# Optimization experiments

Hardware: AMD Instinct MI355X
Metric: run time of the kernel (lower is better)

Reference implementation:

```python
import jax, jax.numpy as jnp
import numpy as np
import math

D_MODEL = 1024
NUM_HEADS = 16
D_K = D_MODEL // NUM_HEADS
B, NQ, NK = 2, 2048, 2048


def setup_inputs() -> dict:
    key = jax.random.key(0)
    ks = jax.random.split(key, 14)
    s = 1.0 / math.sqrt(D_MODEL)
    inp = {
        "query": jax.random.normal(ks[0], (B, NQ, D_MODEL), jnp.float32),
        "key": jax.random.normal(ks[1], (B, NK, D_MODEL), jnp.float32),
        "value": jax.random.normal(ks[2], (B, NK, D_MODEL), jnp.float32),
        "mask": jax.random.randint(ks[3], (B, NK), 0, 2, jnp.int32),
        "attn_bias": jax.random.normal(ks[4], (B, NQ, NK), jnp.float32),
        "w_q": jax.random.normal(ks[5], (D_MODEL, D_MODEL), jnp.float32) * s,
        "b_q": jnp.zeros((D_MODEL,), jnp.float32),
        "w_k": jax.random.normal(ks[6], (D_MODEL, D_MODEL), jnp.float32) * s,
        "b_k": jnp.zeros((D_MODEL,), jnp.float32),
        "w_v": jax.random.normal(ks[7], (D_MODEL, D_MODEL), jnp.float32) * s,
        "b_v": jnp.zeros((D_MODEL,), jnp.float32),
        "w_o": jax.random.normal(ks[8], (D_MODEL, D_MODEL), jnp.float32) * s,
        "b_o": jnp.zeros((D_MODEL,), jnp.float32),
    }
    return inp


def reference(query, key, value, mask, attn_bias, w_q, b_q, w_k, b_k, w_v, b_v, w_o, b_o):
    # Linear projections (torch Linear: x @ W^T + b), reshape to [B, H, N, d_k]
    def proj(x, w, b, n):
        return (x @ w.T + b).reshape(x.shape[0], n, NUM_HEADS, D_K).transpose(0, 2, 1, 3)

    Q = proj(query, w_q, b_q, query.shape[1])   # [B,H,Nq,dk]
    K = proj(key, w_k, b_k, key.shape[1])       # [B,H,Nk,dk]
    V = proj(value, w_v, b_v, value.shape[1])   # [B,H,Nk,dk]

    scores = jnp.einsum("bhqd,bhkd->bhqk", Q, K) / math.sqrt(D_K)
    scores = scores + attn_bias[:, None, :, :]           # bias broadcast over heads
    pad = (mask[:, None, None, :] == 0)                   # [B,1,1,Nk]
    scores = jnp.where(pad, jnp.float32(-1e9), scores)
    attn = jax.nn.softmax(scores, axis=-1)                # dropout is identity (eval)
    out = jnp.einsum("bhqk,bhkd->bhqd", attn, V)          # [B,H,Nq,dk]
    out = out.transpose(0, 2, 1, 3).reshape(query.shape[0], query.shape[1], D_MODEL)
    return out @ w_o.T + b_o
```

## Files before the change

kernel.cpp:

```cpp
#include <hip/hip_runtime.h>


typedef short bf16x8 __attribute__((ext_vector_type(8)));
typedef short bf16x4 __attribute__((ext_vector_type(4)));
typedef float f32x4 __attribute__((ext_vector_type(4)));
typedef float f32x16 __attribute__((ext_vector_type(16)));
typedef int i32x4 __attribute__((ext_vector_type(4)));
typedef unsigned short u16;
typedef unsigned short u16x8 __attribute__((ext_vector_type(8)));
typedef unsigned short u16x4 __attribute__((ext_vector_type(4)));

#define MFMA16(a, b, c) __builtin_amdgcn_mfma_f32_16x16x32_bf16((a), (b), (c), 0, 0, 0)
#define MFMA32(a, b, c) __builtin_amdgcn_mfma_f32_32x32x16_bf16((a), (b), (c), 0, 0, 0)
#define GLD16(gp, lp)                                                     \
  __builtin_amdgcn_global_load_lds(                                       \
      (const __attribute__((address_space(1))) void*)(gp),                \
      (__attribute__((address_space(3))) void*)(lp), 16, 0, 0)

#define WAITVM_BAR(N) asm volatile("s_waitcnt vmcnt(" #N ")\ns_barrier" ::: "memory")
#define BAR() asm volatile("s_barrier" ::: "memory")

#if __has_builtin(__builtin_amdgcn_exp2f)
#define EXP2(x) __builtin_amdgcn_exp2f(x)
#else
#define EXP2(x) exp2f(x)
#endif

__device__ __forceinline__ u16 f2bf(float f) {
  union { float f; unsigned u; } v; v.f = f;
  return (u16)((v.u + 0x7fffu + ((v.u >> 16) & 1u)) >> 16);
}
__device__ __forceinline__ unsigned pk2(float x, float y) {
  union { float f; unsigned u; } a, b;
  a.f = x; b.f = y;
  return ((a.u + 0x8000u) >> 16) | ((b.u + 0x8000u) & 0xffff0000u);
}
__device__ __forceinline__ void pl32swap(unsigned& a, unsigned& b) {
  asm("v_permlane32_swap_b32 %0, %1" : "+v"(a), "+v"(b));
}

struct ConvDesc { const float* src; u16* dst; int n; };
struct ConvArgs { ConvDesc d[7]; };

__device__ __forceinline__ void biasprep_body(const float* __restrict__ bias,
                                              const int* __restrict__ mask,
                                              u16* __restrict__ out, int i) {
  const int o0 = i * 16;
  const int rowg = o0 >> 11;
  const int b = rowg >> 11;
  const int off = o0 & 2047;
  const int c = off >> 5;
  const int hi = (off >> 4) & 1;
  const float* src = bias + (size_t)rowg * 2048 + c * 32 + hi * 4;
  const int* msk = mask + b * 2048 + c * 32 + hi * 4;
  u16x8 w0 = {}, w1 = {};
#pragma unroll
  for (int t = 0; t < 4; t++) {
    f32x4 v = *(const f32x4*)(src + t * 8);
    i32x4 m = *(const i32x4*)(msk + t * 8);
#pragma unroll
    for (int j = 0; j < 4; j++) {
      u16 val = (m[j] != 0) ? f2bf(v[j] * 1.44269504f) : (u16)0xFF80;
      if (t < 2) w0[t * 4 + j] = val;
      else       w1[(t - 2) * 4 + j] = val;
    }
  }
  *(u16x8*)(out + o0) = w0;
  *(u16x8*)(out + o0 + 8) = w1;
}

__global__ __launch_bounds__(256)
void k_prep(ConvArgs a, const float* __restrict__ bias,
            const int* __restrict__ mask, u16* __restrict__ bout) {
  if (blockIdx.y == 7) {
    biasprep_body(bias, mask, bout, blockIdx.x * 256 + threadIdx.x);
    return;
  }
  ConvDesc cd = a.d[blockIdx.y];
  int i = (blockIdx.x * 256 + threadIdx.x) * 8;
  if (i >= cd.n) return;
  const float4* s = (const float4*)(cd.src + i);
  float4 f0 = s[0], f1 = s[1];
  u16x8 o;
  o[0] = f2bf(f0.x); o[1] = f2bf(f0.y); o[2] = f2bf(f0.z); o[3] = f2bf(f0.w);
  o[4] = f2bf(f1.x); o[5] = f2bf(f1.y); o[6] = f2bf(f1.z); o[7] = f2bf(f1.w);
  *(u16x8*)(cd.dst + i) = o;
}

__global__ __launch_bounds__(256)
void k_biasprep(const float* __restrict__ bias, const int* __restrict__ mask,
                u16* __restrict__ out) {
  biasprep_body(bias, mask, out, blockIdx.x * 256 + threadIdx.x);
}

template <int MF>
__device__ __forceinline__ void gemm_impl(const u16* __restrict__ A,
                                          const u16* __restrict__ Bw,
                                          const float* __restrict__ bias,
                                          void* __restrict__ outp, int mode,
                                          float oscale) {
  __shared__ u16 As[2][MF * 1024];
  __shared__ u16 Bs[2][4096];
  const int tid = threadIdx.x;
  const int lane = tid & 63;
  const int wv = tid >> 6;
  const int wr = wv >> 1, wc = wv & 1;
  const int m0 = blockIdx.y * (MF * 32), n0 = blockIdx.x * 128;

  f32x4 acc[MF][4] = {};

  const int s0 = tid, s1 = 256 + tid;
  const int r0 = s0 >> 2, c0 = (s0 & 3) ^ (r0 & 3);
  const int r1 = s1 >> 2, c1 = (s1 & 3) ^ (r1 & 3);
  const u16* gA0 = A + (size_t)(m0 + r0) * 1024 + c0 * 8;
  const u16* gA1 = A + (size_t)(m0 + r1) * 1024 + c1 * 8;
  const u16* gB0 = Bw + (size_t)(n0 + r0) * 1024 + c0 * 8;
  const u16* gB1 = Bw + (size_t)(n0 + r1) * 1024 + c1 * 8;
  u16* lA0 = &As[0][(tid & ~63) * 8];
  u16* lB0 = &Bs[0][(tid & ~63) * 8];

  GLD16(gA0, lA0);
  if constexpr (MF == 4) GLD16(gA1, lA0 + 2048);
  GLD16(gB0, lB0);
  GLD16(gB1, lB0 + 2048);
  WAITVM_BAR(0);

#define GSTEP(BUF, K0)                                                     \
  {                                                                        \
    const int nk = ((K0) + 32) & 1023;                                     \
    GLD16(gA0 + nk, lA0 + ((BUF) ^ 1) * (MF * 1024));                      \
    if constexpr (MF == 4)                                                 \
      GLD16(gA1 + nk, lA0 + 2048 + ((BUF) ^ 1) * (MF * 1024));             \
    GLD16(gB0 + nk, lB0 + ((BUF) ^ 1) * 4096);                             \
    GLD16(gB1 + nk, lB0 + 2048 + ((BUF) ^ 1) * 4096);                      \
    if constexpr (MF == 4) { WAITVM_BAR(4); } else { WAITVM_BAR(3); }      \
    bf16x8 af[MF], bfr[4];                                                 \
    _Pragma("unroll")                                                      \
    for (int mi = 0; mi < MF; mi++) {                                      \
      int row = wr * (MF * 16) + mi * 16 + (lane & 15);                    \
      int byt = row * 64 + (((lane >> 4) * 16) ^ ((row & 3) << 4));        \
      af[mi] = *(const bf16x8*)((const char*)&As[BUF][0] + byt);           \
    }                                                                      \
    _Pragma("unroll")                                                      \
    for (int ni = 0; ni < 4; ni++) {                                       \
      int row = wc * 64 + ni * 16 + (lane & 15);                           \
      int byt = row * 64 + (((lane >> 4) * 16) ^ ((row & 3) << 4));        \
      bfr[ni] = *(const bf16x8*)((const char*)&Bs[BUF][0] + byt);          \
    }                                                                      \
    __builtin_amdgcn_s_setprio(1);                                         \
    _Pragma("unroll")                                                      \
    for (int mi = 0; mi < MF; mi++)                                        \
      _Pragma("unroll")                                                    \
      for (int ni = 0; ni < 4; ni++)                                       \
        acc[mi][ni] = MFMA16(af[mi], bfr[ni], acc[mi][ni]);                \
    __builtin_amdgcn_s_setprio(0);                                         \
    BAR();                                                                 \
  }

  for (int k0 = 0; k0 < 1024; k0 += 64) {
    GSTEP(0, k0)
    GSTEP(1, k0 + 32)
  }
#undef GSTEP

#pragma unroll
  for (int ni = 0; ni < 4; ni++) {
    int n = n0 + wc * 64 + ni * 16 + (lane & 15);
    float bv = bias[n];
#pragma unroll
    for (int mi = 0; mi < MF; mi++) {
      int mb = m0 + wr * (MF * 16) + mi * 16 + (lane >> 4) * 4;
      if (mode == 2) {
        float* O = (float*)outp;
#pragma unroll
        for (int r = 0; r < 4; r++)
          O[(size_t)(mb + r) * 1024 + n] = (acc[mi][ni][r] + bv) * oscale;
      } else if (mode == 0) {
        u16* O = (u16*)outp;
        int b = mb >> 11, q = mb & 2047;
        int h = n >> 6, dk = n & 63;
        size_t base = ((size_t)(b * 16 + h) * 2048 + q) * 64 + dk;
#pragma unroll
        for (int r = 0; r < 4; r++)
          O[base + (size_t)r * 64] = f2bf((acc[mi][ni][r] + bv) * oscale);
      } else {
        u16* O = (u16*)outp;
        int b = mb >> 11, kv = mb & 2047;
        int h = n >> 6, dk = n & 63;
        u16x4 pk;
#pragma unroll
        for (int r = 0; r < 4; r++) pk[r] = f2bf((acc[mi][ni][r] + bv) * oscale);
        *(u16x4*)((u16*)O + ((size_t)((b * 16 + h) * 64 + dk)) * 2048 + kv) = pk;
      }
    }
  }
}

struct GemmDesc { const u16* A; const u16* W; const float* bias; void* out;
                  int mode; float oscale; };
struct Gemm3 { GemmDesc d[3]; };

__global__ __launch_bounds__(256, 2) void k_gemm_qkv(Gemm3 g3) {
  GemmDesc gd = g3.d[blockIdx.z];
  gemm_impl<4>(gd.A, gd.W, gd.bias, gd.out, gd.mode, gd.oscale);
}
__global__ __launch_bounds__(256, 2)
void k_gemm_o(const u16* __restrict__ A, const u16* __restrict__ W,
              const float* __restrict__ bias, float* __restrict__ out) {
  gemm_impl<2>(A, W, bias, out, 2, 1.0f);
}

__global__ __launch_bounds__(256, 2)
void k_attn(const u16* __restrict__ Qb, const u16* __restrict__ Kb,
            const u16* __restrict__ Vt, const u16* __restrict__ BiasE,
            u16* __restrict__ Ob) {
  __shared__ u16 Ks[2][128 * 64];
  __shared__ u16 Vs[2][64 * 128];

  const int tid = threadIdx.x, lane = tid & 63, w = tid >> 6;
  const int l31 = lane & 31, hi2 = lane >> 5;
  const int bid = blockIdx.x;
  const int xcd = bid & 7, rr = bid >> 3;
  const int qt = rr & 15;
  const int pr = xcd + 8 * (rr >> 4);
  const int b = pr >> 4, h = pr & 15;
  const int q0 = qt * 128;
  const size_t bh = (size_t)(b * 16 + h);

  const u16* Qrow = Qb + (bh * 2048 + q0 + w * 32 + l31) * 64 + hi2 * 8;
  bf16x8 bq[4];
#pragma unroll
  for (int dc = 0; dc < 4; dc++) bq[dc] = *(const bf16x8*)(Qrow + dc * 16);

  f32x16 acc[2] = {};
  float mrun = -1e30f, lrun = 0.f;

  const u16* Kg = Kb + bh * 2048 * 64;
  const u16* Vg = Vt + bh * 64 * 2048;
  int rK[4], cK[4], rV[4], cV[4], ldd[4];
#pragma unroll
  for (int i = 0; i < 4; i++) {
    int s = i * 256 + tid;
    rK[i] = s >> 3; cK[i] = (s & 7) ^ (rK[i] & 7);
    rV[i] = s >> 4; cV[i] = (s & 15) ^ (rV[i] & 7);
    ldd[i] = (i * 256 + (tid & ~63)) * 8;
  }
  const int kx = (lane & 7) << 4;

  const u16* brow =
      BiasE + ((size_t)b * 2048 + q0 + w * 32 + l31) * 2048 + hi2 * 16;

#pragma unroll
  for (int i = 0; i < 4; i++)
    GLD16(Kg + (size_t)rK[i] * 64 + cK[i] * 8, &Ks[0][ldd[i]]);
#pragma unroll
  for (int i = 0; i < 4; i++)
    GLD16(Vg + (size_t)rV[i] * 2048 + cV[i] * 8, &Vs[0][ldd[i]]);
  u16x8 bb[4][2];
#pragma unroll
  for (int c = 0; c < 4; c++) {
    bb[c][0] = *(const u16x8*)(brow + c * 32);
    bb[c][1] = *(const u16x8*)(brow + c * 32 + 8);
  }

#define ATTN_STEP(BUF, T)                                                      \
  {                                                                            \
    WAITVM_BAR(0);            \
    const char* kb = (const char*)&Ks[BUF][0];                                 \
    const char* vb = (const char*)&Vs[BUF][0];                                 \
    f32x16 sc[4];                                                              \
    __builtin_amdgcn_s_setprio(1);                                             \
    _Pragma("unroll")                                                          \
    for (int c = 0; c < 4; c++) {                                              \
      f32x16 z;                                                                \
      _Pragma("unroll")                                                        \
      for (int r = 0; r < 8; r++)                                              \
        z[r] = __uint_as_float((unsigned)bb[c][0][r] << 16);                   \
      _Pragma("unroll")                                                        \
      for (int r = 0; r < 8; r++)                                              \
        z[8 + r] = __uint_as_float((unsigned)bb[c][1][r] << 16);               \
      const int rowb = (c * 32 + l31) * 128;                                   \
      _Pragma("unroll")                                                        \
      for (int dc = 0; dc < 4; dc++) {                                         \
        bf16x8 ak =                                                            \
            *(const bf16x8*)(kb + rowb + ((dc * 32 + hi2 * 16) ^ kx));         \
        z = MFMA32(ak, bq[dc], z);                                             \
      }                                                                        \
      sc[c] = z;                                                               \
    }                                                                          \
    __builtin_amdgcn_s_setprio(0);                                             \
    const int nkv = (((T) + 1) & 15) * 128;                                    \
    _Pragma("unroll")                                                          \
    for (int i = 0; i < 4; i++)                                                \
      GLD16(Kg + (size_t)(nkv + rK[i]) * 64 + cK[i] * 8,                       \
            &Ks[(BUF) ^ 1][ldd[i]]);                                           \
    _Pragma("unroll")                                                          \
    for (int i = 0; i < 4; i++)                                                \
      GLD16(Vg + (size_t)rV[i] * 2048 + nkv + cV[i] * 8,                       \
            &Vs[(BUF) ^ 1][ldd[i]]);                                           \
    _Pragma("unroll")                                                          \
    for (int c = 0; c < 4; c++) {                                              \
      bb[c][0] = *(const u16x8*)(brow + nkv + c * 32);                         \
      bb[c][1] = *(const u16x8*)(brow + nkv + c * 32 + 8);                     \
    }                                                                          \
    float tmax = -3e38f;                                                       \
    _Pragma("unroll")                                                          \
    for (int c = 0; c < 4; c++)                                                \
      _Pragma("unroll")                                                        \
      for (int r = 0; r < 16; r++) tmax = fmaxf(tmax, sc[c][r]);               \
    tmax = fmaxf(tmax, __shfl_xor(tmax, 32, 64));                              \
    if (__any(tmax > mrun)) {                                                  \
      float mnew = fmaxf(mrun, tmax);                                          \
      float alpha = EXP2(mrun - mnew);                                         \
      mrun = mnew;                                                             \
      lrun *= alpha;                                                           \
      _Pragma("unroll")                                                        \
      for (int ds = 0; ds < 2; ds++)                                           \
        _Pragma("unroll")                                                      \
        for (int r = 0; r < 16; r++) acc[ds][r] *= alpha;                      \
    }                                                                          \
    float rsum = 0.f;                                                          \
    _Pragma("unroll")                                                          \
    for (int c = 0; c < 4; c++)                                                \
      _Pragma("unroll")                                                        \
      for (int r = 0; r < 16; r++) {                                           \
        sc[c][r] = EXP2(sc[c][r] - mrun);                                      \
        rsum += sc[c][r];                                                      \
      }                                                                        \
    rsum += __shfl_xor(rsum, 32, 64);                                          \
    lrun += rsum;                                                              \
    __builtin_amdgcn_s_setprio(1);                                             \
    _Pragma("unroll")                                                          \
    for (int c = 0; c < 4; c++) {                                              \
      unsigned a0 = pk2(sc[c][0], sc[c][1]), b0 = pk2(sc[c][4], sc[c][5]);     \
      unsigned a1 = pk2(sc[c][2], sc[c][3]), b1 = pk2(sc[c][6], sc[c][7]);     \
      unsigned e0 = pk2(sc[c][8], sc[c][9]), f0 = pk2(sc[c][12], sc[c][13]);   \
      unsigned e1 = pk2(sc[c][10], sc[c][11]), f1 = pk2(sc[c][14], sc[c][15]); \
      pl32swap(a0, b0); pl32swap(a1, b1);                                      \
      pl32swap(e0, f0); pl32swap(e1, f1);                                      \
      union { unsigned u[4]; bf16x8 v; } fe, fo;                               \
      fe.u[0] = a0; fe.u[1] = a1; fe.u[2] = b0; fe.u[3] = b1;                  \
      fo.u[0] = e0; fo.u[1] = e1; fo.u[2] = f0; fo.u[3] = f1;                  \
      _Pragma("unroll")                                                        \
      for (int ds = 0; ds < 2; ds++) {                                         \
        const int vrow = (ds * 32 + l31) * 256;                                \
        bf16x8 ve =                                                            \
            *(const bf16x8*)(vb + vrow + (((c * 4 + hi2) * 16) ^ kx));         \
        acc[ds] = MFMA32(ve, fe.v, acc[ds]);                                   \
        bf16x8 vo =                                                            \
            *(const bf16x8*)(vb + vrow + (((c * 4 + 2 + hi2) * 16) ^ kx));     \
        acc[ds] = MFMA32(vo, fo.v, acc[ds]);                                   \
      }                                                                        \
    }                                                                          \
    __builtin_amdgcn_s_setprio(0);                                             \
  }

  for (int t = 0; t < 16; t += 2) {
    ATTN_STEP(0, t)
    ATTN_STEP(1, t + 1)
  }
#undef ATTN_STEP

  float linv = 1.0f / lrun;
  const size_t obase =
      ((size_t)b * 2048 + q0 + w * 32 + l31) * 1024 + h * 64 + hi2 * 4;
#pragma unroll
  for (int ds = 0; ds < 2; ds++)
#pragma unroll
    for (int t = 0; t < 4; t++) {
      u16x4 pk;
#pragma unroll
      for (int j = 0; j < 4; j++) pk[j] = f2bf(acc[ds][t * 4 + j] * linv);
      *(u16x4*)(Ob + obase + ds * 32 + t * 8) = pk;
    }
}

extern "C" void kernel_launch(void* const* d_in, const int* in_sizes, int n_in,
                              void* d_out, int out_size, void* d_ws,
                              size_t ws_size, hipStream_t stream) {
  (void)in_sizes; (void)n_in; (void)out_size;
  const float* q_in = (const float*)d_in[0];
  const float* k_in = (const float*)d_in[1];
  const float* v_in = (const float*)d_in[2];
  const int* mask = (const int*)d_in[3];
  const float* attn_bias = (const float*)d_in[4];
  const float* w_q = (const float*)d_in[5];
  const float* b_q = (const float*)d_in[6];
  const float* w_k = (const float*)d_in[7];
  const float* b_k = (const float*)d_in[8];
  const float* w_v = (const float*)d_in[9];
  const float* b_v = (const float*)d_in[10];
  const float* w_o = (const float*)d_in[11];
  const float* b_o = (const float*)d_in[12];

  const size_t MB = 1u << 20;
  char* ws = (char*)d_ws;
  u16* XQ = (u16*)(ws + 0 * MB);
  u16* XK = (u16*)(ws + 8 * MB);
  u16* XV = (u16*)(ws + 16 * MB);
  u16* WQ = (u16*)(ws + 24 * MB);
  u16* WK = (u16*)(ws + 26 * MB);
  u16* WV = (u16*)(ws + 28 * MB);
  u16* WO = (u16*)(ws + 30 * MB);
  u16* Qb = (u16*)(ws + 32 * MB);
  u16* Kb = (u16*)(ws + 40 * MB);
  u16* Vt = (u16*)(ws + 48 * MB);
  u16* Ob = (u16*)(ws + 56 * MB);
  const bool merged = ws_size >= (size_t)80 * MB;
  u16* BiasE = (u16*)(ws + (merged ? 64 : 0) * MB);

  ConvArgs ca;
  ca.d[0] = {q_in, XQ, 4096 * 1024};
  ca.d[1] = {k_in, XK, 4096 * 1024};
  ca.d[2] = {v_in, XV, 4096 * 1024};
  ca.d[3] = {w_q, WQ, 1024 * 1024};
  ca.d[4] = {w_k, WK, 1024 * 1024};
  ca.d[5] = {w_v, WV, 1024 * 1024};
  ca.d[6] = {w_o, WO, 1024 * 1024};
  k_prep<<<dim3(2048, merged ? 8 : 7), 256, 0, stream>>>(ca, attn_bias, mask,
                                                         BiasE);

  const float QSCALE = 0.125f * 1.44269504f;
  Gemm3 g3;
  g3.d[0] = {XQ, WQ, b_q, (void*)Qb, 0, QSCALE};
  g3.d[1] = {XK, WK, b_k, (void*)Kb, 0, 1.0f};
  g3.d[2] = {XV, WV, b_v, (void*)Vt, 1, 1.0f};
  k_gemm_qkv<<<dim3(8, 32, 3), 256, 0, stream>>>(g3);

  if (!merged) k_biasprep<<<2048, 256, 0, stream>>>(attn_bias, mask, BiasE);

  k_attn<<<512, 256, 0, stream>>>(Qb, Kb, Vt, BiasE, Ob);

  k_gemm_o<<<dim3(8, 64), 256, 0, stream>>>(Ob, WO, b_o, (float*)d_out);
}
```

Measured before the change: 149.3 us.

## Tune attention softmax: tree reductions, lazy rescale, hardware bf16 pack, QKV occupancy

Several independent tweaks land together. The row-max and row-sum in the attention inner loop become tree reductions using three-input max, which shortens dependency chains. The running-max rescale now fires only when the new max exceeds the old by more than 8 (log2 units), which skips most accumulator rescales but lets exponentials reach up to 2^8 before rescale. Manual bf16 packing is replaced with the HIP __float22bfloat162_rn intrinsic, which may map to a hardware convert instruction. The QKV GEMM launch bound is raised to 3 blocks per SM, which can force register spills.

After: 147.4 us. Within noise of the previous version (-1.2%).

```diff
diff --git a/kernel.cpp b/kernel.cpp
--- a/kernel.cpp
+++ b/kernel.cpp
@@ -1,4 +1,5 @@
 #include <hip/hip_runtime.h>
+#include <hip/hip_bf16.h>
 
 
 typedef short bf16x8 __attribute__((ext_vector_type(8)));
@@ -30,10 +31,10 @@
   union { float f; unsigned u; } v; v.f = f;
   return (u16)((v.u + 0x7fffu + ((v.u >> 16) & 1u)) >> 16);
 }
-__device__ __forceinline__ unsigned pk2(float x, float y) {
-  union { float f; unsigned u; } a, b;
-  a.f = x; b.f = y;
-  return ((a.u + 0x8000u) >> 16) | ((b.u + 0x8000u) & 0xffff0000u);
+__device__ __forceinline__ unsigned pkc(float lo, float hi) {
+  __hip_bfloat162 h = __float22bfloat162_rn(float2{lo, hi});
+  union { __hip_bfloat162 h; unsigned u; } c; c.h = h;
+  return c.u;
 }
 __device__ __forceinline__ void pl32swap(unsigned& a, unsigned& b) {
   asm("v_permlane32_swap_b32 %0, %1" : "+v"(a), "+v"(b));
@@ -200,7 +201,7 @@
                   int mode; float oscale; };
 struct Gemm3 { GemmDesc d[3]; };
 
-__global__ __launch_bounds__(256, 2) void k_gemm_qkv(Gemm3 g3) {
+__global__ __launch_bounds__(256, 3) void k_gemm_qkv(Gemm3 g3) {
   GemmDesc gd = g3.d[blockIdx.z];
   gemm_impl<4>(gd.A, gd.W, gd.bias, gd.out, gd.mode, gd.oscale);
 }
@@ -303,13 +304,20 @@
       bb[c][0] = *(const u16x8*)(brow + nkv + c * 32);                         \
       bb[c][1] = *(const u16x8*)(brow + nkv + c * 32 + 8);                     \
     }                                                                          \
-    float tmax = -3e38f;                                                       \
-    _Pragma("unroll")                                                          \
-    for (int c = 0; c < 4; c++)                                                \
-      _Pragma("unroll")                                                        \
-      for (int r = 0; r < 16; r++) tmax = fmaxf(tmax, sc[c][r]);               \
+    float cm[4];                                                               \
+    _Pragma("unroll")                                                          \
+    for (int c = 0; c < 4; c++) {     \
+      float qa = fmaxf(fmaxf(sc[c][0], sc[c][1]), sc[c][2]);                   \
+      float qb = fmaxf(fmaxf(sc[c][3], sc[c][4]), sc[c][5]);                   \
+      float qc = fmaxf(fmaxf(sc[c][6], sc[c][7]), sc[c][8]);                   \
+      float qd = fmaxf(fmaxf(sc[c][9], sc[c][10]), sc[c][11]);                 \
+      float qe = fmaxf(fmaxf(sc[c][12], sc[c][13]), sc[c][14]);                \
+      cm[c] = fmaxf(fmaxf(fmaxf(qa, qb), fmaxf(qc, qd)),                       \
+                    fmaxf(qe, sc[c][15]));                                     \
+    }                                                                          \
+    float tmax = fmaxf(fmaxf(cm[0], cm[1]), fmaxf(cm[2], cm[3]));              \
     tmax = fmaxf(tmax, __shfl_xor(tmax, 32, 64));                              \
-    if (__any(tmax > mrun)) {                                                  \
+    if (__any(tmax > mrun + 8.f)) {           \
       float mnew = fmaxf(mrun, tmax);                                          \
       float alpha = EXP2(mrun - mnew);                                         \
       mrun = mnew;                                                             \
@@ -319,23 +327,31 @@
         _Pragma("unroll")                                                      \
         for (int r = 0; r < 16; r++) acc[ds][r] *= alpha;                      \
     }                                                                          \
-    float rsum = 0.f;                                                          \
     _Pragma("unroll")                                                          \
     for (int c = 0; c < 4; c++)                                                \
       _Pragma("unroll")                                                        \
-      for (int r = 0; r < 16; r++) {                                           \
-        sc[c][r] = EXP2(sc[c][r] - mrun);                                      \
-        rsum += sc[c][r];                                                      \
-      }                                                                        \
+      for (int r = 0; r < 16; r++) sc[c][r] = EXP2(sc[c][r] - mrun);           \
+    float cs[4];                                                               \
+    _Pragma("unroll")                                                          \
+    for (int c = 0; c < 4; c++) {                                              \
+      float s8[8];                                                             \
+      _Pragma("unroll")                                                        \
+      for (int r = 0; r < 8; r++) s8[r] = sc[c][r] + sc[c][r + 8];             \
+      float s4[4];                                                             \
+      _Pragma("unroll")                                                        \
+      for (int r = 0; r < 4; r++) s4[r] = s8[r] + s8[r + 4];                   \
+      cs[c] = (s4[0] + s4[1]) + (s4[2] + s4[3]);                               \
+    }                                                                          \
+    float rsum = (cs[0] + cs[1]) + (cs[2] + cs[3]);                            \
     rsum += __shfl_xor(rsum, 32, 64);                                          \
     lrun += rsum;                                                              \
     __builtin_amdgcn_s_setprio(1);                                             \
     _Pragma("unroll")                                                          \
     for (int c = 0; c < 4; c++) {                                              \
-      unsigned a0 = pk2(sc[c][0], sc[c][1]), b0 = pk2(sc[c][4], sc[c][5]);     \
-      unsigned a1 = pk2(sc[c][2], sc[c][3]), b1 = pk2(sc[c][6], sc[c][7]);     \
-      unsigned e0 = pk2(sc[c][8], sc[c][9]), f0 = pk2(sc[c][12], sc[c][13]);   \
-      unsigned e1 = pk2(sc[c][10], sc[c][11]), f1 = pk2(sc[c][14], sc[c][15]); \
+      unsigned a0 = pkc(sc[c][0], sc[c][1]), b0 = pkc(sc[c][4], sc[c][5]);     \
+      unsigned a1 = pkc(sc[c][2], sc[c][3]), b1 = pkc(sc[c][6], sc[c][7]);     \
+      unsigned e0 = pkc(sc[c][8], sc[c][9]), f0 = pkc(sc[c][12], sc[c][13]);   \
+      unsigned e1 = pkc(sc[c][10], sc[c][11]), f1 = pkc(sc[c][14], sc[c][15]); \
       pl32swap(a0, b0); pl32swap(a1, b1);                                      \
       pl32swap(e0, f0); pl32swap(e1, f1);                                      \
       union { unsigned u[4]; bf16x8 v; } fe, fo;                               \
```
